# Kernel optimization log

Hardware: AMD Instinct MI355X
Metric: run time of the kernel (lower is better)

## Reference

```python
import jax, jax.numpy as jnp
import numpy as np

B, L, E, H = 4, 2048, 1024, 16
DK = E // H


def setup_inputs() -> dict:
    key = jax.random.key(0)
    k1, k2, k3 = jax.random.split(key, 3)
    x = jax.random.normal(k1, (B, L, E), dtype=jnp.float32)
    # torch Linear weights are [out, in]; xavier-ish scaling
    w_qkv = jax.random.normal(k2, (3 * E, E), dtype=jnp.float32) * (2.0 / (E + 3 * E)) ** 0.5
    wo = jax.random.normal(k3, (E, E), dtype=jnp.float32) * (1.0 / E) ** 0.5
    # causal mask: scores filled with -inf where mask == 0
    mask = jnp.tril(jnp.ones((L, L), dtype=bool))
    return {"x": x, "mask": mask, "w_qkv": w_qkv, "wo": wo}


def reference(x, mask, w_qkv, wo):
    b, l, e = x.shape
    # qkv projection: Linear with weight [3E, E] -> x @ W^T
    qkv = x @ w_qkv.T                              # [b, l, 3E]
    qkv = qkv.reshape(b, l, 3, H, DK)              # (three h d) split
    q = jnp.transpose(qkv[:, :, 0], (0, 2, 1, 3))  # [b, h, l, d]
    k = jnp.transpose(qkv[:, :, 1], (0, 2, 1, 3))
    v = jnp.transpose(qkv[:, :, 2], (0, 2, 1, 3))
    scores = jnp.einsum('bhld,bhmd->bhlm', q, k) / np.sqrt(DK)  # [b, h, l, l]
    scores = jnp.where(mask, scores, -jnp.inf)
    attn = jax.nn.softmax(scores, axis=-1)
    out = jnp.einsum('bhlm,bhmd->bhld', attn, v)   # [b, h, l, d]
    out = jnp.transpose(out, (0, 2, 1, 3)).reshape(b, l, e)  # b l (h d)
    return out @ wo.T
```

## Files before the change

kernel.cpp:

```cpp
#include <hip/hip_runtime.h>
#include <stdint.h>


typedef __bf16 bf16;
typedef __bf16 bf16x4 __attribute__((ext_vector_type(4)));
typedef __bf16 bf16x8 __attribute__((ext_vector_type(8)));
typedef float floatx4 __attribute__((ext_vector_type(4)));
typedef short s16x4 __attribute__((ext_vector_type(4)));

#define MFMA32(a, b, c) __builtin_amdgcn_mfma_f32_16x16x32_bf16(a, b, c, 0, 0, 0)
#define MFMA16(a, b, c) __builtin_amdgcn_mfma_f32_16x16x16bf16_1k(a, b, c, 0, 0, 0)

typedef const __attribute__((address_space(1))) uint32_t* gas_t;
typedef __attribute__((address_space(3))) uint32_t* las_t;

__device__ __forceinline__ void async16(void* lds, const void* g) {
  __builtin_amdgcn_global_load_lds((gas_t)g, (las_t)lds, 16, 0, 0);
}

__global__ void cvt_all(const float4* __restrict__ x, const float4* __restrict__ wq,
                        const float4* __restrict__ wo, bf16x4* __restrict__ xb,
                        bf16x4* __restrict__ wqb, bf16x4* __restrict__ wob) {
  const int NX = 2097152, NQ = 786432;
  int i = blockIdx.x * blockDim.x + threadIdx.x;
  float4 v;
  bf16x4* dst;
  int j;
  if (i < NX) { j = i; v = x[j]; dst = xb; }
  else if (i < NX + NQ) { j = i - NX; v = wq[j]; dst = wqb; }
  else { j = i - NX - NQ; v = wo[j]; dst = wob; }
  bf16x4 o;
  o[0] = (bf16)v.x; o[1] = (bf16)v.y; o[2] = (bf16)v.z; o[3] = (bf16)v.w;
  dst[j] = o;
}

template <int MODE>
__global__ __launch_bounds__(256) void gemm_bt(
    const bf16* __restrict__ A, const bf16* __restrict__ B,
    float* __restrict__ Cf, bf16* __restrict__ Qb, bf16* __restrict__ Kb,
    bf16* __restrict__ Vt, int M, int N, int K) {
  __shared__ __align__(16) bf16 smem[128 * 136];
  bf16* As = smem;
  bf16* Bs = smem + 128 * 32;
  const int tid = threadIdx.x;
  const int wave = tid >> 6, lane = tid & 63;
  const int wm = wave & 1, wn = wave >> 1;
  const int row0 = blockIdx.y * 128, col0 = blockIdx.x * 128;
  const int l15 = lane & 15, quad = lane >> 4;
  const int srow = lane >> 2;
  const int scol = (lane & 3) * 8;

  floatx4 acc[4][4] = {};

  for (int k0 = 0; k0 < K; k0 += 32) {
#pragma unroll
    for (int i = 0; i < 2; ++i) {
      int c = wave + i * 4;
      async16(&As[c * 512], A + (size_t)(row0 + c * 16 + srow) * K + k0 + scol);
      async16(&Bs[c * 512], B + (size_t)(col0 + c * 16 + srow) * K + k0 + scol);
    }
    __syncthreads();
    bf16x8 af[4], bfr[4];
#pragma unroll
    for (int t = 0; t < 4; ++t) {
      af[t]  = *(const bf16x8*)&As[(wm * 64 + t * 16 + l15) * 32 + quad * 8];
      bfr[t] = *(const bf16x8*)&Bs[(wn * 64 + t * 16 + l15) * 32 + quad * 8];
    }
#pragma unroll
    for (int mt = 0; mt < 4; ++mt)
#pragma unroll
      for (int nt = 0; nt < 4; ++nt)
        acc[mt][nt] = MFMA32(af[mt], bfr[nt], acc[mt][nt]);
    __syncthreads();
  }

  if (MODE == 1 && col0 >= 2048) {
#pragma unroll
    for (int mt = 0; mt < 4; ++mt)
#pragma unroll
      for (int nt = 0; nt < 4; ++nt) {
        int nl = wn * 64 + nt * 16 + l15;
        int ll = wm * 64 + mt * 16 + quad * 4;
        bf16x4 t;
#pragma unroll
        for (int r = 0; r < 4; ++r) t[r] = (bf16)acc[mt][nt][r];
        *(bf16x4*)&smem[nl * 136 + ll] = t;
      }
    __syncthreads();
    const int bb = row0 >> 11, l_base = row0 & 2047, hd0 = col0 - 2048;
#pragma unroll
    for (int it = 0; it < 8; ++it) {
      int rowi = it * 16 + (tid >> 4);
      int li = (tid & 15) * 8;
      bf16x8 v = *(const bf16x8*)&smem[rowi * 136 + li];
      int hd = hd0 + rowi;
      *(bf16x8*)&Vt[((((size_t)bb * 16 + (hd >> 6)) * 64 + (hd & 63)) << 11) +
                    l_base + li] = v;
    }
    return;
  }

#pragma unroll
  for (int mt = 0; mt < 4; ++mt)
#pragma unroll
    for (int nt = 0; nt < 4; ++nt)
#pragma unroll
      for (int r = 0; r < 4; ++r) {
        int gr = row0 + wm * 64 + mt * 16 + quad * 4 + r;
        int gc = col0 + wn * 64 + nt * 16 + l15;
        float v = acc[mt][nt][r];
        if (MODE == 2) {
          Cf[(size_t)gr * N + gc] = v;
        } else {
          int t = gc >> 10, hd = gc & 1023;
          if (t == 0) Qb[(size_t)gr * 1024 + hd] = (bf16)v;
          else        Kb[(size_t)gr * 1024 + hd] = (bf16)v;
        }
      }
}

__global__ __launch_bounds__(256) void gemm2_64(
    const bf16* __restrict__ A, const bf16* __restrict__ B,
    float* __restrict__ Cf, int M, int N, int K) {
  __shared__ __align__(16) bf16 As[64 * 32];
  __shared__ __align__(16) bf16 Bs[128 * 32];
  const int tid = threadIdx.x;
  const int wave = tid >> 6, lane = tid & 63;
  const int row0 = blockIdx.y * 64, col0 = blockIdx.x * 128;
  const int l15 = lane & 15, quad = lane >> 4;
  const int srow = lane >> 2, scol = (lane & 3) * 8;

  floatx4 acc[4][2] = {};

  for (int k0 = 0; k0 < K; k0 += 32) {
#pragma unroll
    for (int i = 0; i < 3; ++i) {
      int c = wave * 3 + i;
      if (c < 4)
        async16(&As[c * 512], A + (size_t)(row0 + c * 16 + srow) * K + k0 + scol);
      else
        async16(&Bs[(c - 4) * 512],
                B + (size_t)(col0 + (c - 4) * 16 + srow) * K + k0 + scol);
    }
    __syncthreads();
    bf16x8 af[4], bfr[2];
#pragma unroll
    for (int t = 0; t < 4; ++t)
      af[t] = *(const bf16x8*)&As[(t * 16 + l15) * 32 + quad * 8];
#pragma unroll
    for (int t = 0; t < 2; ++t)
      bfr[t] = *(const bf16x8*)&Bs[(wave * 32 + t * 16 + l15) * 32 + quad * 8];
#pragma unroll
    for (int mt = 0; mt < 4; ++mt)
#pragma unroll
      for (int nt = 0; nt < 2; ++nt)
        acc[mt][nt] = MFMA32(af[mt], bfr[nt], acc[mt][nt]);
    __syncthreads();
  }

#pragma unroll
  for (int mt = 0; mt < 4; ++mt)
#pragma unroll
    for (int nt = 0; nt < 2; ++nt)
#pragma unroll
      for (int r = 0; r < 4; ++r) {
        int gr = row0 + mt * 16 + quad * 4 + r;
        int gc = col0 + wave * 32 + nt * 16 + l15;
        Cf[(size_t)gr * N + gc] = acc[mt][nt][r];
      }
}

__global__ __launch_bounds__(256, 2) void flash_attn(
    const bf16* __restrict__ Qb, const bf16* __restrict__ Kb,
    const bf16* __restrict__ Vt, bf16* __restrict__ Ob) {
  const int bid = blockIdx.x;
  const int pr = bid & 15;
  const int bh = bid >> 4;
  const int b = bh >> 4, h = bh & 15;
  const int tid = threadIdx.x;
  const int wave = tid >> 6, lane = tid & 63;
  const int l15 = lane & 15, quad = lane >> 4;

  const int qA = pr, qB = 31 - pr;
  const int ktA = qA >> 1, ktB = qB >> 1;

  __shared__ __align__(16) bf16 Ks[128 * 64];
  __shared__ __align__(16) bf16 Vs[64 * 128];

  const size_t x_base = (size_t)b * 2048 * 1024 + (size_t)h * 64;
  const size_t vt_base = (size_t)bh * 64 * 2048;

  auto load_q = [&](int q64, bf16x8* qf) {
#pragma unroll
    for (int ks = 0; ks < 2; ++ks) {
      const bf16* p = Qb + x_base +
          (size_t)(q64 * 64 + wave * 16 + l15) * 1024 + ks * 32 + quad * 8;
      bf16x8 v = *(const bf16x8*)p;
#pragma unroll
      for (int j = 0; j < 8; ++j) v[j] = (bf16)((float)v[j] * 0.18033688f);
      qf[ks] = v;
    }
  };
  bf16x8 qfA[2], qfB[2];
  load_q(qA, qfA);
  load_q(qB, qfB);

  floatx4 oA[4] = {}, oB[4] = {};
  float lA = 0.f, lB = 0.f;

  const int k_lr = lane >> 3, k_c = lane & 7;
  const int v_lr = lane >> 4, v_c = lane & 15;

  auto process = [&](const bf16x8* qf, floatx4* o, float& l_run,
                     int kt, int q64, bool diag) {
    floatx4 s[8] = {};
#pragma unroll
    for (int nt = 0; nt < 8; ++nt) {
      int krow = nt * 16 + l15;
#pragma unroll
      for (int ks = 0; ks < 2; ++ks) {
        bf16x8 kf = *(const bf16x8*)&Ks[krow * 64 + ((((ks << 2) | quad) ^ (l15 & 7)) << 3)];
        s[nt] = MFMA32(kf, qf[ks], s[nt]);
      }
    }
    if (diag) {
      int q_g = q64 * 64 + wave * 16 + l15;
#pragma unroll
      for (int nt = 0; nt < 8; ++nt)
#pragma unroll
        for (int r = 0; r < 4; ++r)
          if (kt * 128 + nt * 16 + quad * 4 + r > q_g) s[nt][r] = -__builtin_inff();
    }
    float ls = 0.f;
#pragma unroll
    for (int nt = 0; nt < 8; ++nt)
#pragma unroll
      for (int r = 0; r < 4; ++r) {
        float p = exp2f(s[nt][r]);
        s[nt][r] = p;
        ls += p;
      }
    l_run += ls;

#pragma unroll
    for (int kb = 0; kb < 8; ++kb) {
      int c16 = (((kb << 1) | (quad >> 1)) ^ l15) & 15;
      s16x4 vf[4];
#pragma unroll
      for (int dt = 0; dt < 4; ++dt)
        vf[dt] = *(const s16x4*)&Vs[(dt * 16 + l15) * 128 + (c16 << 3) + ((quad & 1) << 2)];
      bf16x4 pb;
#pragma unroll
      for (int r = 0; r < 4; ++r) pb[r] = (bf16)s[kb][r];
      s16x4 pf = __builtin_bit_cast(s16x4, pb);
#pragma unroll
      for (int dt = 0; dt < 4; ++dt)
        o[dt] = MFMA16(vf[dt], pf, o[dt]);
    }
  };

  for (int kt = 0; kt <= ktB; ++kt) {
#pragma unroll
    for (int i = 0; i < 4; ++i) {
      int o8 = wave * 4 + i;
      int krow = o8 * 8 + k_lr;
      async16(&Ks[o8 * 512],
              Kb + x_base + (size_t)(kt * 128 + krow) * 1024 + ((k_c ^ (krow & 7)) << 3));
      int vrow = o8 * 4 + v_lr;
      async16(&Vs[o8 * 512],
              Vt + vt_base + (size_t)vrow * 2048 + kt * 128 + ((v_c ^ (vrow & 15)) << 3));
    }
    __syncthreads();

    process(qfB, oB, lB, kt, qB, kt == ktB);
    if (kt <= ktA) process(qfA, oA, lA, kt, qA, kt == ktA);

    __syncthreads();
  }

  auto store_o = [&](const floatx4* o, float l_run, int q64) {
    float lf = l_run;
    lf += __shfl_xor(lf, 16);
    lf += __shfl_xor(lf, 32);
    float inv = 1.0f / lf;
    size_t rowoff = x_base + (size_t)(q64 * 64 + wave * 16 + l15) * 1024;
#pragma unroll
    for (int dt = 0; dt < 4; ++dt) {
      bf16x4 ob;
#pragma unroll
      for (int r = 0; r < 4; ++r) ob[r] = (bf16)(o[dt][r] * inv);
      *(bf16x4*)(Ob + rowoff + dt * 16 + quad * 4) = ob;
    }
  };
  store_o(oA, lA, qA);
  store_o(oB, lB, qB);
}

extern "C" void kernel_launch(void* const* d_in, const int* in_sizes, int n_in,
                              void* d_out, int out_size, void* d_ws, size_t ws_size,
                              hipStream_t stream) {
  const float* x     = (const float*)d_in[0];
  const float* w_qkv = (const float*)d_in[2];
  const float* wo    = (const float*)d_in[3];
  float* out = (float*)d_out;

  char* ws = (char*)d_ws;
  bf16* xb  = (bf16*)(ws);
  bf16* wqb = (bf16*)(ws + (16u << 20));
  bf16* wob = (bf16*)(ws + (22u << 20));
  bf16* Qb  = (bf16*)(ws + (24u << 20));
  bf16* Kb  = (bf16*)(ws + (40u << 20));
  bf16* Vt  = (bf16*)(ws + (56u << 20));
  bf16* Ab  = (bf16*)(ws);

  cvt_all<<<12288, 256, 0, stream>>>((const float4*)x, (const float4*)w_qkv,
                                     (const float4*)wo, (bf16x4*)xb,
                                     (bf16x4*)wqb, (bf16x4*)wob);

  gemm_bt<1><<<dim3(24, 64), 256, 0, stream>>>(xb, wqb, nullptr, Qb, Kb, Vt,
                                               8192, 3072, 1024);
  flash_attn<<<1024, 256, 0, stream>>>(Qb, Kb, Vt, Ab);
  gemm2_64<<<dim3(8, 128), 256, 0, stream>>>(Ab, wob, out, 8192, 1024, 1024);
}
```

Baseline: 289.6 us.

## Double-buffer 64-wide K/V tiles in flash attention with async prefetch

Shrinks the key tile from 128 to 64 rows and double-buffers the K and V tiles in LDS. The next tile is prefetched asynchronously while the current one is computed, replacing the load-sync-compute-sync pattern with one barrier per iteration. It also raises wave priority around the MFMA sections with s_setprio. The smaller tiles mean more iterations and barriers and shorter MFMA bursts, and correctness of the prefetch depends on the barrier covering the async loads.

Measured after the change: 278.9 us. 1.04x faster.

```diff
diff --git a/kernel.cpp b/kernel.cpp
--- a/kernel.cpp
+++ b/kernel.cpp
@@ -182,13 +182,29 @@
   const int l15 = lane & 15, quad = lane >> 4;
 
   const int qA = pr, qB = 31 - pr;
-  const int ktA = qA >> 1, ktB = qB >> 1;
-
-  __shared__ __align__(16) bf16 Ks[128 * 64];
-  __shared__ __align__(16) bf16 Vs[64 * 128];
+
+  __shared__ __align__(16) bf16 Ks2[2 * 64 * 64];
+  __shared__ __align__(16) bf16 Vs2[2 * 64 * 64];
 
   const size_t x_base = (size_t)b * 2048 * 1024 + (size_t)h * 64;
   const size_t vt_base = (size_t)bh * 64 * 2048;
+
+  const int k_lr = lane >> 3, k_c = lane & 7;
+
+  auto stage = [&](int kt, int bufsel) {
+    bf16* Kd = Ks2 + bufsel * 4096;
+    bf16* Vd = Vs2 + bufsel * 4096;
+#pragma unroll
+    for (int i = 0; i < 2; ++i) {
+      int o8 = wave * 2 + i;
+      int row = o8 * 8 + k_lr;
+      int sw = (k_c ^ (row & 7)) << 3;
+      async16(&Kd[o8 * 512],
+              Kb + x_base + (size_t)(kt * 64 + row) * 1024 + sw);
+      async16(&Vd[o8 * 512],
+              Vt + vt_base + (size_t)row * 2048 + kt * 64 + sw);
+    }
+  };
 
   auto load_q = [&](int q64, bf16x8* qf) {
 #pragma unroll
@@ -201,6 +217,9 @@
       qf[ks] = v;
     }
   };
+
+  stage(0, 0);
+
   bf16x8 qfA[2], qfB[2];
   load_q(qA, qfA);
   load_q(qB, qfB);
@@ -208,32 +227,32 @@
   floatx4 oA[4] = {}, oB[4] = {};
   float lA = 0.f, lB = 0.f;
 
-  const int k_lr = lane >> 3, k_c = lane & 7;
-  const int v_lr = lane >> 4, v_c = lane & 15;
-
   auto process = [&](const bf16x8* qf, floatx4* o, float& l_run,
-                     int kt, int q64, bool diag) {
-    floatx4 s[8] = {};
-#pragma unroll
-    for (int nt = 0; nt < 8; ++nt) {
+                     int kt, int q64, bool diag, const bf16* Ks, const bf16* Vs) {
+    floatx4 s[4] = {};
+    __builtin_amdgcn_s_setprio(1);
+#pragma unroll
+    for (int nt = 0; nt < 4; ++nt) {
       int krow = nt * 16 + l15;
 #pragma unroll
       for (int ks = 0; ks < 2; ++ks) {
-        bf16x8 kf = *(const bf16x8*)&Ks[krow * 64 + ((((ks << 2) | quad) ^ (l15 & 7)) << 3)];
+        bf16x8 kf = *(const bf16x8*)&Ks[krow * 64 +
+            ((((ks << 2) | quad) ^ (l15 & 7)) << 3)];
         s[nt] = MFMA32(kf, qf[ks], s[nt]);
       }
     }
+    __builtin_amdgcn_s_setprio(0);
     if (diag) {
       int q_g = q64 * 64 + wave * 16 + l15;
 #pragma unroll
-      for (int nt = 0; nt < 8; ++nt)
+      for (int nt = 0; nt < 4; ++nt)
 #pragma unroll
         for (int r = 0; r < 4; ++r)
-          if (kt * 128 + nt * 16 + quad * 4 + r > q_g) s[nt][r] = -__builtin_inff();
+          if (kt * 64 + nt * 16 + quad * 4 + r > q_g) s[nt][r] = -__builtin_inff();
     }
     float ls = 0.f;
 #pragma unroll
-    for (int nt = 0; nt < 8; ++nt)
+    for (int nt = 0; nt < 4; ++nt)
 #pragma unroll
       for (int r = 0; r < 4; ++r) {
         float p = exp2f(s[nt][r]);
@@ -242,40 +261,34 @@
       }
     l_run += ls;
 
-#pragma unroll
-    for (int kb = 0; kb < 8; ++kb) {
-      int c16 = (((kb << 1) | (quad >> 1)) ^ l15) & 15;
-      s16x4 vf[4];
-#pragma unroll
-      for (int dt = 0; dt < 4; ++dt)
-        vf[dt] = *(const s16x4*)&Vs[(dt * 16 + l15) * 128 + (c16 << 3) + ((quad & 1) << 2)];
+    __builtin_amdgcn_s_setprio(1);
+#pragma unroll
+    for (int kb = 0; kb < 4; ++kb) {
       bf16x4 pb;
 #pragma unroll
       for (int r = 0; r < 4; ++r) pb[r] = (bf16)s[kb][r];
       s16x4 pf = __builtin_bit_cast(s16x4, pb);
 #pragma unroll
-      for (int dt = 0; dt < 4; ++dt)
-        o[dt] = MFMA16(vf[dt], pf, o[dt]);
-    }
+      for (int dt = 0; dt < 4; ++dt) {
+        s16x4 vf = *(const s16x4*)&Vs[(dt * 16 + l15) * 64 +
+            (((((kb << 1) | (quad >> 1)) ^ (l15 & 7))) << 3) + ((quad & 1) << 2)];
+        o[dt] = MFMA16(vf, pf, o[dt]);
+      }
+    }
+    __builtin_amdgcn_s_setprio(0);
   };
 
-  for (int kt = 0; kt <= ktB; ++kt) {
-#pragma unroll
-    for (int i = 0; i < 4; ++i) {
-      int o8 = wave * 4 + i;
-      int krow = o8 * 8 + k_lr;
-      async16(&Ks[o8 * 512],
-              Kb + x_base + (size_t)(kt * 128 + krow) * 1024 + ((k_c ^ (krow & 7)) << 3));
-      int vrow = o8 * 4 + v_lr;
-      async16(&Vs[o8 * 512],
-              Vt + vt_base + (size_t)vrow * 2048 + kt * 128 + ((v_c ^ (vrow & 15)) << 3));
-    }
-    __syncthreads();
-
-    process(qfB, oB, lB, kt, qB, kt == ktB);
-    if (kt <= ktA) process(qfA, oA, lA, kt, qA, kt == ktA);
-
-    __syncthreads();
+  __syncthreads();
+
+  int cur = 0;
+  for (int kt = 0; kt <= qB; ++kt) {
+    if (kt < qB) stage(kt + 1, cur ^ 1);
+    const bf16* Kc = Ks2 + cur * 4096;
+    const bf16* Vc = Vs2 + cur * 4096;
+    process(qfB, oB, lB, kt, qB, kt == qB, Kc, Vc);
+    if (kt <= qA) process(qfA, oA, lA, kt, qA, kt == qA, Kc, Vc);
+    __syncthreads();
+    cur ^= 1;
   }
 
   auto store_o = [&](const floatx4* o, float l_run, int q64) {
```
